# Performance work log

Measured on AMD Instinct MI355X. Metric: run time of the kernel, lower is better.

Reference implementation:

```python
import jax, jax.numpy as jnp
import numpy as np

CROP_H, CROP_W = 7, 7

def _sample_coords(lo, hi, extent, n):
    # TF crop_and_resize: coord = lo*(extent-1) + i*(hi-lo)*(extent-1)/(n-1)
    step = (hi - lo) * (extent - 1) / (n - 1)          # [N]
    return lo[:, None] * (extent - 1) + jnp.arange(n, dtype=lo.dtype)[None, :] * step[:, None]  # [N, n]

def crop_and_resize(image, boxes, box_ind, crop_h, crop_w):
    # image: [B,H,W,C], boxes: [N,4] normalized (y1,x1,y2,x2), box_ind: [N]
    B, H, W, C = image.shape
    y1, x1, y2, x2 = boxes[:, 0], boxes[:, 1], boxes[:, 2], boxes[:, 3]
    ys = _sample_coords(y1, y2, H, crop_h)             # [N, crop_h]
    xs = _sample_coords(x1, x2, W, crop_w)             # [N, crop_w]

    y0 = jnp.floor(ys); x0 = jnp.floor(xs)
    wy = (ys - y0)[:, :, None, None]                    # [N,ch,1,1] lerp weight
    wx = (xs - x0)[:, None, :, None]                    # [N,1,cw,1]
    y0i = jnp.clip(y0.astype(jnp.int32), 0, H - 1)
    y1i = jnp.clip(y0i + 1, 0, H - 1)
    x0i = jnp.clip(x0.astype(jnp.int32), 0, W - 1)
    x1i = jnp.clip(x0i + 1, 0, W - 1)

    b = box_ind[:, None, None]                          # [N,1,1]
    def corner(yi, xi):                                 # -> [N,ch,cw,C]
        return image[b, yi[:, :, None], xi[:, None, :]]

    top = corner(y0i, x0i) + (corner(y0i, x1i) - corner(y0i, x0i)) * wx
    bot = corner(y1i, x0i) + (corner(y1i, x1i) - corner(y1i, x0i)) * wx
    out = top + (bot - top) * wy                        # [N,ch,cw,C]

    # TF uses extrapolation_value=0 for samples outside the image
    vy = ((ys >= 0) & (ys <= H - 1))[:, :, None, None]
    vx = ((xs >= 0) & (xs <= W - 1))[:, None, :, None]
    return jnp.where(vy & vx, out, jnp.zeros((), out.dtype))


def setup_inputs() -> dict:
    key = jax.random.key(0)
    k1, k2, k3 = jax.random.split(key, 3)
    feats = jax.random.normal(k1, (8, 64, 64, 256), dtype=jnp.float32)
    boxes = jax.random.uniform(k2, (4000, 4), dtype=jnp.float32)
    box_ind = jax.random.randint(k3, (4000, 1), 0, 8, dtype=jnp.int32)
    return {"feats": feats, "boxes": boxes, "box_ind": box_ind}


def reference(feats, boxes, box_ind):
    ind = box_ind.reshape(-1)
    return crop_and_resize(feats, boxes, ind, CROP_H, CROP_W)
```

## Files before the change

kernel.cpp:

```cpp
#include <hip/hip_runtime.h>


#define H 64
#define W 64
#define C 256
#define CROP_HW 49
#define NIMG 8
#define G 8

typedef float f32x4 __attribute__((ext_vector_type(4)));

__global__ __launch_bounds__(512) void bucket_kernel(
    const int* __restrict__ box_ind,
    int* __restrict__ order,
    int* __restrict__ offsets,
    int n)
{
    const int wave = threadIdx.x >> 6;
    const int lane = threadIdx.x & 63;
    __shared__ int counts[NIMG];

    int cnt = 0;
    for (int i = lane; i < n; i += 64)
        cnt += (box_ind[i] == wave);
    for (int off = 32; off; off >>= 1)
        cnt += __shfl_down(cnt, off);
    if (lane == 0) counts[wave] = cnt;
    __syncthreads();

    int start = 0;
    for (int i = 0; i < wave; ++i) start += counts[i];
    if (threadIdx.x == 0) {
        int acc = 0;
        for (int i = 0; i < NIMG; ++i) { offsets[i] = acc; acc += counts[i]; }
        offsets[NIMG] = acc;
    }

    int pos = start;
    for (int base = 0; base < n; base += 64) {
        const int i = base + lane;
        const bool m = (i < n) && (box_ind[i] == wave);
        const unsigned long long mask = __ballot(m);
        const int below = __popcll(mask & ((1ULL << lane) - 1ULL));
        if (m) order[pos + below] = i;
        pos += __popcll(mask);
    }
}

struct Cell {
    int p00, p01, p10, p11;
    float wx, wy;
    bool valid;
    int oidx;
};

__device__ __forceinline__ Cell cell_info(
    int c, const int* __restrict__ order, const f32x4* __restrict__ boxes4,
    int start)
{
    Cell k;
    const int bi = c / CROP_HW;
    const int r  = c - bi * CROP_HW;
    const int iy = r / 7;
    const int ix = r - iy * 7;
    const int b  = order[start + bi];

    const f32x4 bx = boxes4[b];

    const float stepy = (bx.z - bx.x) * 63.0f / 6.0f;
    const float stepx = (bx.w - bx.y) * 63.0f / 6.0f;
    const float ys = bx.x * 63.0f + (float)iy * stepy;
    const float xs = bx.y * 63.0f + (float)ix * stepx;

    const float y0f = floorf(ys);
    const float x0f = floorf(xs);
    k.wy = ys - y0f;
    k.wx = xs - x0f;

    const int y0 = min(max((int)y0f, 0), H - 1);
    const int y1 = min(y0 + 1, H - 1);
    const int x0 = min(max((int)x0f, 0), W - 1);
    const int x1 = min(x0 + 1, W - 1);

    k.valid = (ys >= 0.0f) && (ys <= (float)(H - 1)) &&
              (xs >= 0.0f) && (xs <= (float)(W - 1));

    k.p00 = y0 * W + x0;
    k.p01 = y0 * W + x1;
    k.p10 = y1 * W + x0;
    k.p11 = y1 * W + x1;

    k.oidx = (b * CROP_HW + r) * (C / 4);
    return k;
}

__global__ __launch_bounds__(256, 4) void crop_resize_xcd(
    const float* __restrict__ feats,
    const float* __restrict__ boxes,
    const int*   __restrict__ order,
    const int*   __restrict__ offsets,
    float*       __restrict__ out)
{
    const int img  = blockIdx.x & 7;
    const int slot = blockIdx.x >> 3;
    const int lane = threadIdx.x & 63;
    const int wv   = threadIdx.x >> 6;

    const int start   = offsets[img];
    const int nb      = offsets[img + 1] - start;
    const int ncells  = nb * CROP_HW;
    const int ngroups = (ncells + G - 1) / G;
    const int wave_local = slot * 4 + wv;
    const int stride     = (gridDim.x >> 3) * 4;

    const f32x4* __restrict__ f4 = reinterpret_cast<const f32x4*>(feats)
                                   + (size_t)img * (H * W * (C / 4));
    const f32x4* __restrict__ boxes4 = reinterpret_cast<const f32x4*>(boxes);
    f32x4* __restrict__ o4 = reinterpret_cast<f32x4*>(out);

    for (int gi = wave_local; gi < ngroups; gi += stride) {
        const int cbase = gi * G;
        const int nval  = min(G, ncells - cbase);

        int c = cbase + (lane & (G - 1));
        if (c > ncells - 1) c = ncells - 1;
        const Cell k = cell_info(c, order, boxes4, start);
        const unsigned long long vmask = __ballot(k.valid);

        #pragma unroll
        for (int j = 0; j < G; ++j) {
            if (j >= nval) break;
            const int   s00 = __builtin_amdgcn_readlane(k.p00, j);
            const int   s01 = __builtin_amdgcn_readlane(k.p01, j);
            const int   s10 = __builtin_amdgcn_readlane(k.p10, j);
            const int   s11 = __builtin_amdgcn_readlane(k.p11, j);
            const float swx = __uint_as_float(
                __builtin_amdgcn_readlane(__float_as_uint(k.wx), j));
            const float swy = __uint_as_float(
                __builtin_amdgcn_readlane(__float_as_uint(k.wy), j));
            const int   sox = __builtin_amdgcn_readlane(k.oidx, j);
            const bool  sval = (vmask >> j) & 1ULL;

            const f32x4 v00 = f4[s00 * (C / 4) + lane];
            const f32x4 v01 = f4[s01 * (C / 4) + lane];
            const f32x4 v10 = f4[s10 * (C / 4) + lane];
            const f32x4 v11 = f4[s11 * (C / 4) + lane];

            const float w11 = swx * swy;
            const float w01 = swx - w11;
            const float w10 = swy - w11;
            const float w00 = 1.0f - swx - swy + w11;

            f32x4 res = v00 * w00;
            res += v01 * w01;
            res += v10 * w10;
            res += v11 * w11;
            if (!sval) res = (f32x4)0.0f;

            __builtin_nontemporal_store(res, &o4[sox + lane]);
        }
    }
}

extern "C" void kernel_launch(void* const* d_in, const int* in_sizes, int n_in,
                              void* d_out, int out_size, void* d_ws, size_t ws_size,
                              hipStream_t stream) {
    const float* feats   = (const float*)d_in[0];
    const float* boxes   = (const float*)d_in[1];
    const int*   box_ind = (const int*)d_in[2];
    float*       out     = (float*)d_out;

    const int n_boxes = in_sizes[1] / 4;

    int* order   = (int*)d_ws;
    int* offsets = order + n_boxes;

    bucket_kernel<<<1, 512, 0, stream>>>(box_ind, order, offsets, n_boxes);

    crop_resize_xcd<<<2048, 256, 0, stream>>>(feats, boxes, order, offsets, out);
}
```

Baseline: 70.38 us.

## Convert features to bf16 in a prep pass and gather from bf16 copy

```diff
diff --git a/kernel.cpp b/kernel.cpp
--- a/kernel.cpp
+++ b/kernel.cpp
@@ -8,42 +8,65 @@
 #define NIMG 8
 #define G 8
 
-typedef float f32x4 __attribute__((ext_vector_type(4)));
-
-__global__ __launch_bounds__(512) void bucket_kernel(
-    const int* __restrict__ box_ind,
+typedef float          f32x4 __attribute__((ext_vector_type(4)));
+typedef unsigned short u16x4 __attribute__((ext_vector_type(4)));
+typedef unsigned int   u32x2 __attribute__((ext_vector_type(2)));
+
+__device__ __forceinline__ unsigned short f2bf(float f) {
+    unsigned u = __float_as_uint(f);
+    unsigned r = (u + 0x7fffu + ((u >> 16) & 1u)) >> 16;
+    return (unsigned short)r;
+}
+
+__global__ __launch_bounds__(512) void prep_kernel(
+    const int*   __restrict__ box_ind,
+    const float* __restrict__ feats,
     int* __restrict__ order,
     int* __restrict__ offsets,
-    int n)
-{
-    const int wave = threadIdx.x >> 6;
-    const int lane = threadIdx.x & 63;
-    __shared__ int counts[NIMG];
-
-    int cnt = 0;
-    for (int i = lane; i < n; i += 64)
-        cnt += (box_ind[i] == wave);
-    for (int off = 32; off; off >>= 1)
-        cnt += __shfl_down(cnt, off);
-    if (lane == 0) counts[wave] = cnt;
-    __syncthreads();
-
-    int start = 0;
-    for (int i = 0; i < wave; ++i) start += counts[i];
-    if (threadIdx.x == 0) {
-        int acc = 0;
-        for (int i = 0; i < NIMG; ++i) { offsets[i] = acc; acc += counts[i]; }
-        offsets[NIMG] = acc;
-    }
-
-    int pos = start;
-    for (int base = 0; base < n; base += 64) {
-        const int i = base + lane;
-        const bool m = (i < n) && (box_ind[i] == wave);
-        const unsigned long long mask = __ballot(m);
-        const int below = __popcll(mask & ((1ULL << lane) - 1ULL));
-        if (m) order[pos + below] = i;
-        pos += __popcll(mask);
+    unsigned short* __restrict__ featsb,
+    int n, int n4)
+{
+    if (blockIdx.x == 0) {
+        const int wave = threadIdx.x >> 6;
+        const int lane = threadIdx.x & 63;
+        __shared__ int counts[NIMG];
+
+        int cnt = 0;
+        for (int i = lane; i < n; i += 64)
+            cnt += (box_ind[i] == wave);
+        for (int off = 32; off; off >>= 1)
+            cnt += __shfl_down(cnt, off);
+        if (lane == 0) counts[wave] = cnt;
+        __syncthreads();
+
+        int start = 0;
+        for (int i = 0; i < wave; ++i) start += counts[i];
+        if (threadIdx.x == 0) {
+            int acc = 0;
+            for (int i = 0; i < NIMG; ++i) { offsets[i] = acc; acc += counts[i]; }
+            offsets[NIMG] = acc;
+        }
+
+        int pos = start;
+        for (int base = 0; base < n; base += 64) {
+            const int i = base + lane;
+            const bool m = (i < n) && (box_ind[i] == wave);
+            const unsigned long long mask = __ballot(m);
+            const int below = __popcll(mask & ((1ULL << lane) - 1ULL));
+            if (m) order[pos + below] = i;
+            pos += __popcll(mask);
+        }
+    } else {
+        const f32x4* __restrict__ in4 = reinterpret_cast<const f32x4*>(feats);
+        u16x4* __restrict__ ob = reinterpret_cast<u16x4*>(featsb);
+        int i = (blockIdx.x - 1) * blockDim.x + threadIdx.x;
+        const int stride = (gridDim.x - 1) * blockDim.x;
+        for (; i < n4; i += stride) {
+            const f32x4 v = in4[i];
+            u16x4 r;
+            r.x = f2bf(v.x); r.y = f2bf(v.y); r.z = f2bf(v.z); r.w = f2bf(v.w);
+            ob[i] = r;
+        }
     }
 }
 
@@ -94,8 +117,17 @@
     return k;
 }
 
-__global__ __launch_bounds__(256, 4) void crop_resize_xcd(
-    const float* __restrict__ feats,
+__device__ __forceinline__ f32x4 bf4_to_f32(u32x2 u) {
+    f32x4 r;
+    r.x = __uint_as_float(u.x << 16);
+    r.y = __uint_as_float(u.x & 0xffff0000u);
+    r.z = __uint_as_float(u.y << 16);
+    r.w = __uint_as_float(u.y & 0xffff0000u);
+    return r;
+}
+
+__global__ __launch_bounds__(256, 4) void crop_resize_bf16(
+    const unsigned short* __restrict__ featsb,
     const float* __restrict__ boxes,
     const int*   __restrict__ order,
     const int*   __restrict__ offsets,
@@ -113,7 +145,7 @@
     const int wave_local = slot * 4 + wv;
     const int stride     = (gridDim.x >> 3) * 4;
 
-    const f32x4* __restrict__ f4 = reinterpret_cast<const f32x4*>(feats)
+    const u32x2* __restrict__ f2 = reinterpret_cast<const u32x2*>(featsb)
                                    + (size_t)img * (H * W * (C / 4));
     const f32x4* __restrict__ boxes4 = reinterpret_cast<const f32x4*>(boxes);
     f32x4* __restrict__ o4 = reinterpret_cast<f32x4*>(out);
@@ -141,6 +173,74 @@
             const int   sox = __builtin_amdgcn_readlane(k.oidx, j);
             const bool  sval = (vmask >> j) & 1ULL;
 
+            const u32x2 u00 = f2[s00 * (C / 4) + lane];
+            const u32x2 u01 = f2[s01 * (C / 4) + lane];
+            const u32x2 u10 = f2[s10 * (C / 4) + lane];
+            const u32x2 u11 = f2[s11 * (C / 4) + lane];
+
+            const float w11 = swx * swy;
+            const float w01 = swx - w11;
+            const float w10 = swy - w11;
+            const float w00 = 1.0f - swx - swy + w11;
+
+            f32x4 res = bf4_to_f32(u00) * w00;
+            res += bf4_to_f32(u01) * w01;
+            res += bf4_to_f32(u10) * w10;
+            res += bf4_to_f32(u11) * w11;
+            if (!sval) res = (f32x4)0.0f;
+
+            __builtin_nontemporal_store(res, &o4[(size_t)sox + lane]);
+        }
+    }
+}
+
+__global__ __launch_bounds__(256, 4) void crop_resize_f32(
+    const float* __restrict__ feats,
+    const float* __restrict__ boxes,
+    const int*   __restrict__ order,
+    const int*   __restrict__ offsets,
+    float*       __restrict__ out)
+{
+    const int img  = blockIdx.x & 7;
+    const int slot = blockIdx.x >> 3;
+    const int lane = threadIdx.x & 63;
+    const int wv   = threadIdx.x >> 6;
+
+    const int start   = offsets[img];
+    const int nb      = offsets[img + 1] - start;
+    const int ncells  = nb * CROP_HW;
+    const int ngroups = (ncells + G - 1) / G;
+    const int wave_local = slot * 4 + wv;
+    const int stride     = (gridDim.x >> 3) * 4;
+
+    const f32x4* __restrict__ f4 = reinterpret_cast<const f32x4*>(feats)
+                                   + (size_t)img * (H * W * (C / 4));
+    const f32x4* __restrict__ boxes4 = reinterpret_cast<const f32x4*>(boxes);
+    f32x4* __restrict__ o4 = reinterpret_cast<f32x4*>(out);
+
+    for (int gi = wave_local; gi < ngroups; gi += stride) {
+        const int cbase = gi * G;
+        const int nval  = min(G, ncells - cbase);
+
+        int c = cbase + (lane & (G - 1));
+        if (c > ncells - 1) c = ncells - 1;
+        const Cell k = cell_info(c, order, boxes4, start);
+        const unsigned long long vmask = __ballot(k.valid);
+
+        #pragma unroll
+        for (int j = 0; j < G; ++j) {
+            if (j >= nval) break;
+            const int   s00 = __builtin_amdgcn_readlane(k.p00, j);
+            const int   s01 = __builtin_amdgcn_readlane(k.p01, j);
+            const int   s10 = __builtin_amdgcn_readlane(k.p10, j);
+            const int   s11 = __builtin_amdgcn_readlane(k.p11, j);
+            const float swx = __uint_as_float(
+                __builtin_amdgcn_readlane(__float_as_uint(k.wx), j));
+            const float swy = __uint_as_float(
+                __builtin_amdgcn_readlane(__float_as_uint(k.wy), j));
+            const int   sox = __builtin_amdgcn_readlane(k.oidx, j);
+            const bool  sval = (vmask >> j) & 1ULL;
+
             const f32x4 v00 = f4[s00 * (C / 4) + lane];
             const f32x4 v01 = f4[s01 * (C / 4) + lane];
             const f32x4 v10 = f4[s10 * (C / 4) + lane];
@@ -157,7 +257,7 @@
             res += v11 * w11;
             if (!sval) res = (f32x4)0.0f;
 
-            __builtin_nontemporal_store(res, &o4[sox + lane]);
+            __builtin_nontemporal_store(res, &o4[(size_t)sox + lane]);
         }
     }
 }
@@ -171,11 +271,24 @@
     float*       out     = (float*)d_out;
 
     const int n_boxes = in_sizes[1] / 4;
+    const int n_feats = in_sizes[0];
 
     int* order   = (int*)d_ws;
     int* offsets = order + n_boxes;
-
-    bucket_kernel<<<1, 512, 0, stream>>>(box_ind, order, offsets, n_boxes);
-
-    crop_resize_xcd<<<2048, 256, 0, stream>>>(feats, boxes, order, offsets, out);
-}
+    const size_t bf_off   = 64 * 1024;
+    const size_t bf_bytes = (size_t)n_feats * 2;
+    unsigned short* featsb = (unsigned short*)((char*)d_ws + bf_off);
+
+    if (ws_size >= bf_off + bf_bytes) {
+        prep_kernel<<<1025, 512, 0, stream>>>(box_ind, feats, order, offsets,
+                                              featsb, n_boxes, n_feats / 4);
+        crop_resize_bf16<<<2048, 256, 0, stream>>>(featsb, boxes, order,
+                                                   offsets, out);
+    } else {
+        prep_kernel<<<1, 512, 0, stream>>>(box_ind, feats, order, offsets,
+                                           (unsigned short*)order ,
+                                           n_boxes, 0);
+        crop_resize_f32<<<2048, 256, 0, stream>>>(feats, boxes, order,
+                                                  offsets, out);
+    }
+}
```

Measured after the change: 73.97 us. 5.1% more time.

## Gather from packed bf16 horizontal-pair shadow and fuse bucketing into crop kernel

Applied to the files above, without the earlier changes.

```diff
diff --git a/kernel.cpp b/kernel.cpp
--- a/kernel.cpp
+++ b/kernel.cpp
@@ -7,63 +7,79 @@
 #define CROP_HW 49
 #define NIMG 8
 #define G 8
-
-typedef float f32x4 __attribute__((ext_vector_type(4)));
-
-__global__ __launch_bounds__(512) void bucket_kernel(
-    const int* __restrict__ box_ind,
-    int* __restrict__ order,
-    int* __restrict__ offsets,
-    int n)
-{
-    const int wave = threadIdx.x >> 6;
-    const int lane = threadIdx.x & 63;
-    __shared__ int counts[NIMG];
-
-    int cnt = 0;
-    for (int i = lane; i < n; i += 64)
-        cnt += (box_ind[i] == wave);
-    for (int off = 32; off; off >>= 1)
-        cnt += __shfl_down(cnt, off);
-    if (lane == 0) counts[wave] = cnt;
-    __syncthreads();
-
-    int start = 0;
-    for (int i = 0; i < wave; ++i) start += counts[i];
-    if (threadIdx.x == 0) {
-        int acc = 0;
-        for (int i = 0; i < NIMG; ++i) { offsets[i] = acc; acc += counts[i]; }
-        offsets[NIMG] = acc;
-    }
-
-    int pos = start;
-    for (int base = 0; base < n; base += 64) {
-        const int i = base + lane;
-        const bool m = (i < n) && (box_ind[i] == wave);
-        const unsigned long long mask = __ballot(m);
-        const int below = __popcll(mask & ((1ULL << lane) - 1ULL));
-        if (m) order[pos + below] = i;
-        pos += __popcll(mask);
+#define MAXB 4096
+
+typedef float        f32x4 __attribute__((ext_vector_type(4)));
+typedef unsigned int u32x4 __attribute__((ext_vector_type(4)));
+
+__device__ __forceinline__ unsigned f2bf(float f) {
+    const unsigned u = __float_as_uint(f);
+    return (u + 0x7fffu + ((u >> 16) & 1u)) >> 16;
+}
+__device__ __forceinline__ unsigned packpair(float a, float b) {
+    return f2bf(a) | (f2bf(b) << 16);
+}
+__device__ __forceinline__ f32x4 lopart(u32x4 u) {
+    f32x4 r;
+    r.x = __uint_as_float(u.x << 16);
+    r.y = __uint_as_float(u.y << 16);
+    r.z = __uint_as_float(u.z << 16);
+    r.w = __uint_as_float(u.w << 16);
+    return r;
+}
+__device__ __forceinline__ f32x4 hipart(u32x4 u) {
+    f32x4 r;
+    r.x = __uint_as_float(u.x & 0xffff0000u);
+    r.y = __uint_as_float(u.y & 0xffff0000u);
+    r.z = __uint_as_float(u.z & 0xffff0000u);
+    r.w = __uint_as_float(u.w & 0xffff0000u);
+    return r;
+}
+
+__global__ __launch_bounds__(256) void build_shadow(
+    const float* __restrict__ feats, unsigned int* __restrict__ shadow)
+{
+    const int img = blockIdx.x & 7;
+    const int blk = blockIdx.x >> 3;
+    const f32x4* __restrict__ in4 =
+        reinterpret_cast<const f32x4*>(feats) + (size_t)img * (H * W * (C / 4));
+    u32x4* __restrict__ o4 =
+        reinterpret_cast<u32x4*>(shadow) + (size_t)img * (H * W * (C / 4));
+
+    int t = blk * 1024 + threadIdx.x;
+    #pragma unroll
+    for (int it = 0; it < 4; ++it, t += 256) {
+        const int l   = t & (C / 4 - 1);
+        const int px  = t >> 6;
+        const int x   = px & (W - 1);
+        const int pxp = (x < W - 1) ? px + 1 : px;
+        const f32x4 a = in4[px  * (C / 4) + l];
+        const f32x4 b = in4[pxp * (C / 4) + l];
+        u32x4 r;
+        r.x = packpair(a.x, b.x);
+        r.y = packpair(a.y, b.y);
+        r.z = packpair(a.z, b.z);
+        r.w = packpair(a.w, b.w);
+        o4[t] = r;
     }
 }
 
 struct Cell {
-    int p00, p01, p10, p11;
+    int p0, p1;
     float wx, wy;
     bool valid;
     int oidx;
 };
 
 __device__ __forceinline__ Cell cell_info(
-    int c, const int* __restrict__ order, const f32x4* __restrict__ boxes4,
-    int start)
+    int c, const int* s_order, const f32x4* __restrict__ boxes4)
 {
     Cell k;
     const int bi = c / CROP_HW;
     const int r  = c - bi * CROP_HW;
     const int iy = r / 7;
     const int ix = r - iy * 7;
-    const int b  = order[start + bi];
+    const int b  = s_order[bi];
 
     const f32x4 bx = boxes4[b];
 
@@ -80,40 +96,59 @@
     const int y0 = min(max((int)y0f, 0), H - 1);
     const int y1 = min(y0 + 1, H - 1);
     const int x0 = min(max((int)x0f, 0), W - 1);
-    const int x1 = min(x0 + 1, W - 1);
 
     k.valid = (ys >= 0.0f) && (ys <= (float)(H - 1)) &&
               (xs >= 0.0f) && (xs <= (float)(W - 1));
 
-    k.p00 = y0 * W + x0;
-    k.p01 = y0 * W + x1;
-    k.p10 = y1 * W + x0;
-    k.p11 = y1 * W + x1;
+    k.p0 = y0 * W + x0;
+    k.p1 = y1 * W + x0;
 
     k.oidx = (b * CROP_HW + r) * (C / 4);
     return k;
 }
 
-__global__ __launch_bounds__(256, 4) void crop_resize_xcd(
-    const float* __restrict__ feats,
+__device__ __forceinline__ int block_bucket(
+    const int* __restrict__ box_ind, int nbox, int img, int lane, int wv,
+    int* s_order, int* s_nb)
+{
+    if (wv == 0) {
+        int pos = 0;
+        for (int base = 0; base < nbox; base += 64) {
+            const int i = base + lane;
+            const bool m = (i < nbox) && (box_ind[i] == img);
+            const unsigned long long mask = __ballot(m);
+            const int below = __popcll(mask & ((1ULL << lane) - 1ULL));
+            if (m) s_order[pos + below] = i;
+            pos += __popcll(mask);
+        }
+        if (lane == 0) *s_nb = pos;
+    }
+    __syncthreads();
+    return *s_nb;
+}
+
+__global__ __launch_bounds__(256, 4) void crop_pair(
+    const unsigned int* __restrict__ shadow,
     const float* __restrict__ boxes,
-    const int*   __restrict__ order,
-    const int*   __restrict__ offsets,
-    float*       __restrict__ out)
+    const int*   __restrict__ box_ind,
+    float*       __restrict__ out,
+    int nbox)
 {
     const int img  = blockIdx.x & 7;
     const int slot = blockIdx.x >> 3;
     const int lane = threadIdx.x & 63;
     const int wv   = threadIdx.x >> 6;
 
-    const int start   = offsets[img];
-    const int nb      = offsets[img + 1] - start;
+    __shared__ int s_order[MAXB];
+    __shared__ int s_nb;
+    const int nb = block_bucket(box_ind, nbox, img, lane, wv, s_order, &s_nb);
+
     const int ncells  = nb * CROP_HW;
     const int ngroups = (ncells + G - 1) / G;
     const int wave_local = slot * 4 + wv;
     const int stride     = (gridDim.x >> 3) * 4;
 
-    const f32x4* __restrict__ f4 = reinterpret_cast<const f32x4*>(feats)
+    const u32x4* __restrict__ pf = reinterpret_cast<const u32x4*>(shadow)
                                    + (size_t)img * (H * W * (C / 4));
     const f32x4* __restrict__ boxes4 = reinterpret_cast<const f32x4*>(boxes);
     f32x4* __restrict__ o4 = reinterpret_cast<f32x4*>(out);
@@ -124,16 +159,14 @@
 
         int c = cbase + (lane & (G - 1));
         if (c > ncells - 1) c = ncells - 1;
-        const Cell k = cell_info(c, order, boxes4, start);
+        const Cell k = cell_info(c, s_order, boxes4);
         const unsigned long long vmask = __ballot(k.valid);
 
         #pragma unroll
         for (int j = 0; j < G; ++j) {
             if (j >= nval) break;
-            const int   s00 = __builtin_amdgcn_readlane(k.p00, j);
-            const int   s01 = __builtin_amdgcn_readlane(k.p01, j);
-            const int   s10 = __builtin_amdgcn_readlane(k.p10, j);
-            const int   s11 = __builtin_amdgcn_readlane(k.p11, j);
+            const int   p0  = __builtin_amdgcn_readlane(k.p0, j);
+            const int   p1  = __builtin_amdgcn_readlane(k.p1, j);
             const float swx = __uint_as_float(
                 __builtin_amdgcn_readlane(__float_as_uint(k.wx), j));
             const float swy = __uint_as_float(
@@ -141,10 +174,80 @@
             const int   sox = __builtin_amdgcn_readlane(k.oidx, j);
             const bool  sval = (vmask >> j) & 1ULL;
 
-            const f32x4 v00 = f4[s00 * (C / 4) + lane];
-            const f32x4 v01 = f4[s01 * (C / 4) + lane];
-            const f32x4 v10 = f4[s10 * (C / 4) + lane];
-            const f32x4 v11 = f4[s11 * (C / 4) + lane];
+            const u32x4 r0 = pf[p0 * (C / 4) + lane];
+            const u32x4 r1 = pf[p1 * (C / 4) + lane];
+
+            const float w11 = swx * swy;
+            const float w01 = swx - w11;
+            const float w10 = swy - w11;
+            const float w00 = 1.0f - swx - swy + w11;
+
+            f32x4 res = lopart(r0) * w00;
+            res += hipart(r0) * w01;
+            res += lopart(r1) * w10;
+            res += hipart(r1) * w11;
+            if (!sval) res = (f32x4)0.0f;
+
+            __builtin_nontemporal_store(res, &o4[(size_t)sox + lane]);
+        }
+    }
+}
+
+__global__ __launch_bounds__(256, 4) void crop_f32(
+    const float* __restrict__ feats,
+    const float* __restrict__ boxes,
+    const int*   __restrict__ box_ind,
+    float*       __restrict__ out,
+    int nbox)
+{
+    const int img  = blockIdx.x & 7;
+    const int slot = blockIdx.x >> 3;
+    const int lane = threadIdx.x & 63;
+    const int wv   = threadIdx.x >> 6;
+
+    __shared__ int s_order[MAXB];
+    __shared__ int s_nb;
+    const int nb = block_bucket(box_ind, nbox, img, lane, wv, s_order, &s_nb);
+
+    const int ncells  = nb * CROP_HW;
+    const int ngroups = (ncells + G - 1) / G;
+    const int wave_local = slot * 4 + wv;
+    const int stride     = (gridDim.x >> 3) * 4;
+
+    const f32x4* __restrict__ f4 = reinterpret_cast<const f32x4*>(feats)
+                                   + (size_t)img * (H * W * (C / 4));
+    const f32x4* __restrict__ boxes4 = reinterpret_cast<const f32x4*>(boxes);
+    f32x4* __restrict__ o4 = reinterpret_cast<f32x4*>(out);
+
+    for (int gi = wave_local; gi < ngroups; gi += stride) {
+        const int cbase = gi * G;
+        const int nval  = min(G, ncells - cbase);
+
+        int c = cbase + (lane & (G - 1));
+        if (c > ncells - 1) c = ncells - 1;
+        const Cell k = cell_info(c, s_order, boxes4);
+        const unsigned long long vmask = __ballot(k.valid);
+
+        #pragma unroll
+        for (int j = 0; j < G; ++j) {
+            if (j >= nval) break;
+            const int   p0  = __builtin_amdgcn_readlane(k.p0, j);
+            const int   p1  = __builtin_amdgcn_readlane(k.p1, j);
+            const float swx = __uint_as_float(
+                __builtin_amdgcn_readlane(__float_as_uint(k.wx), j));
+            const float swy = __uint_as_float(
+                __builtin_amdgcn_readlane(__float_as_uint(k.wy), j));
+            const int   sox = __builtin_amdgcn_readlane(k.oidx, j);
+            const bool  sval = (vmask >> j) & 1ULL;
+
+            const int x00 = p0 & (W - 1);
+            const int p0b = (x00 < W - 1) ? p0 + 1 : p0;
+            const int p1b = (x00 < W - 1) ? p1 + 1 : p1;
+
+            const f32x4 v00 = f4[p0  * (C / 4) + lane];
+            const f32x4 v01 = f4[p0b * (C / 4) + lane];
+            const f32x4 v10 = f4[p1  * (C / 4) + lane];
+            const f32x4 v11 = f4[p1b * (C / 4) + lane];
 
             const float w11 = swx * swy;
             const float w01 = swx - w11;
@@ -157,7 +260,7 @@
             res += v11 * w11;
             if (!sval) res = (f32x4)0.0f;
 
-            __builtin_nontemporal_store(res, &o4[sox + lane]);
+            __builtin_nontemporal_store(res, &o4[(size_t)sox + lane]);
         }
     }
 }
@@ -171,11 +274,17 @@
     float*       out     = (float*)d_out;
 
     const int n_boxes = in_sizes[1] / 4;
-
-    int* order   = (int*)d_ws;
-    int* offsets = order + n_boxes;
-
-    bucket_kernel<<<1, 512, 0, stream>>>(box_ind, order, offsets, n_boxes);
-
-    crop_resize_xcd<<<2048, 256, 0, stream>>>(feats, boxes, order, offsets, out);
-}
+    const int n_feats = in_sizes[0];
+
+    const size_t shadow_bytes = (size_t)n_feats * 4;
+    unsigned int* shadow = (unsigned int*)d_ws;
+
+    if (n_boxes <= MAXB && ws_size >= shadow_bytes) {
+        build_shadow<<<2048, 256, 0, stream>>>(feats, shadow);
+        crop_pair<<<2048, 256, 0, stream>>>(shadow, boxes, box_ind, out, n_boxes);
+    } else if (n_boxes <= MAXB) {
+        crop_f32<<<2048, 256, 0, stream>>>(feats, boxes, box_ind, out, n_boxes);
+    } else {
+        crop_f32<<<2048, 256, 0, stream>>>(feats, boxes, box_ind, out, MAXB);
+    }
+}
```

After: 77.48 us. +10.1%, slower.

## Split block into producer waves computing and consumer waves storing via LDS

Applied to the files above, without the earlier changes.

```diff
diff --git a/kernel.cpp b/kernel.cpp
--- a/kernel.cpp
+++ b/kernel.cpp
@@ -6,7 +6,7 @@
 #define C 256
 #define CROP_HW 49
 #define NIMG 8
-#define G 8
+#define TILE 16
 
 typedef float f32x4 __attribute__((ext_vector_type(4)));
 
@@ -94,7 +94,7 @@
     return k;
 }
 
-__global__ __launch_bounds__(256, 4) void crop_resize_xcd(
+__global__ __launch_bounds__(256, 4) void crop_pc(
     const float* __restrict__ feats,
     const float* __restrict__ boxes,
     const int*   __restrict__ order,
@@ -106,59 +106,76 @@
     const int lane = threadIdx.x & 63;
     const int wv   = threadIdx.x >> 6;
 
-    const int start   = offsets[img];
-    const int nb      = offsets[img + 1] - start;
-    const int ncells  = nb * CROP_HW;
-    const int ngroups = (ncells + G - 1) / G;
-    const int wave_local = slot * 4 + wv;
-    const int stride     = (gridDim.x >> 3) * 4;
+    const int start  = offsets[img];
+    const int nb     = offsets[img + 1] - start;
+    const int ncells = nb * CROP_HW;
+    const int ntiles = (ncells + TILE - 1) / TILE;
+    const int nslots = gridDim.x >> 3;
 
     const f32x4* __restrict__ f4 = reinterpret_cast<const f32x4*>(feats)
                                    + (size_t)img * (H * W * (C / 4));
     const f32x4* __restrict__ boxes4 = reinterpret_cast<const f32x4*>(boxes);
     f32x4* __restrict__ o4 = reinterpret_cast<f32x4*>(out);
 
-    for (int gi = wave_local; gi < ngroups; gi += stride) {
-        const int cbase = gi * G;
-        const int nval  = min(G, ncells - cbase);
+    __shared__ f32x4 buf[TILE][64];
+    __shared__ int   oid[TILE];
 
-        int c = cbase + (lane & (G - 1));
-        if (c > ncells - 1) c = ncells - 1;
-        const Cell k = cell_info(c, order, boxes4, start);
-        const unsigned long long vmask = __ballot(k.valid);
+    for (int t = slot; t < ntiles; t += nslots) {
+        const int cbase = t * TILE;
 
-        #pragma unroll
-        for (int j = 0; j < G; ++j) {
-            if (j >= nval) break;
-            const int   s00 = __builtin_amdgcn_readlane(k.p00, j);
-            const int   s01 = __builtin_amdgcn_readlane(k.p01, j);
-            const int   s10 = __builtin_amdgcn_readlane(k.p10, j);
-            const int   s11 = __builtin_amdgcn_readlane(k.p11, j);
-            const float swx = __uint_as_float(
-                __builtin_amdgcn_readlane(__float_as_uint(k.wx), j));
-            const float swy = __uint_as_float(
-                __builtin_amdgcn_readlane(__float_as_uint(k.wy), j));
-            const int   sox = __builtin_amdgcn_readlane(k.oidx, j);
-            const bool  sval = (vmask >> j) & 1ULL;
+        if (wv < 2) {
+            int c = cbase + wv * 8 + (lane & 7);
+            if (c > ncells - 1) c = ncells - 1;
+            const Cell k = cell_info(c, order, boxes4, start);
+            const unsigned long long vmask = __ballot(k.valid);
 
-            const f32x4 v00 = f4[s00 * (C / 4) + lane];
-            const f32x4 v01 = f4[s01 * (C / 4) + lane];
-            const f32x4 v10 = f4[s10 * (C / 4) + lane];
-            const f32x4 v11 = f4[s11 * (C / 4) + lane];
+            if (lane < 8) oid[wv * 8 + lane] = k.oidx;
 
-            const float w11 = swx * swy;
-            const float w01 = swx - w11;
-            const float w10 = swy - w11;
-            const float w00 = 1.0f - swx - swy + w11;
+            #pragma unroll
+            for (int j = 0; j < 8; ++j) {
+                const int   s00 = __builtin_amdgcn_readlane(k.p00, j);
+                const int   s01 = __builtin_amdgcn_readlane(k.p01, j);
+                const int   s10 = __builtin_amdgcn_readlane(k.p10, j);
+                const int   s11 = __builtin_amdgcn_readlane(k.p11, j);
+                const float swx = __uint_as_float(
+                    __builtin_amdgcn_readlane(__float_as_uint(k.wx), j));
+                const float swy = __uint_as_float(
+                    __builtin_amdgcn_readlane(__float_as_uint(k.wy), j));
+                const bool  sval = (vmask >> j) & 1ULL;
 
-            f32x4 res = v00 * w00;
-            res += v01 * w01;
-            res += v10 * w10;
-            res += v11 * w11;
-            if (!sval) res = (f32x4)0.0f;
+                const f32x4 v00 = f4[s00 * (C / 4) + lane];
+                const f32x4 v01 = f4[s01 * (C / 4) + lane];
+                const f32x4 v10 = f4[s10 * (C / 4) + lane];
+                const f32x4 v11 = f4[s11 * (C / 4) + lane];
 
-            __builtin_nontemporal_store(res, &o4[sox + lane]);
+                const float w11 = swx * swy;
+                const float w01 = swx - w11;
+                const float w10 = swy - w11;
+                const float w00 = 1.0f - swx - swy + w11;
+
+                f32x4 res = v00 * w00;
+                res += v01 * w01;
+                res += v10 * w10;
+                res += v11 * w11;
+                if (!sval) res = (f32x4)0.0f;
+
+                buf[wv * 8 + j][lane] = res;
+            }
         }
+
+        __syncthreads();
+
+        if (wv >= 2) {
+            #pragma unroll
+            for (int j = 0; j < 8; ++j) {
+                const int row = (wv - 2) * 8 + j;
+                const f32x4 res = buf[row][lane];
+                const int   ox  = oid[row];
+                __builtin_nontemporal_store(res, &o4[(size_t)ox + lane]);
+            }
+        }
+
+        __syncthreads();
     }
 }
 
@@ -177,5 +194,5 @@
 
     bucket_kernel<<<1, 512, 0, stream>>>(box_ind, order, offsets, n_boxes);
 
-    crop_resize_xcd<<<2048, 256, 0, stream>>>(feats, boxes, order, offsets, out);
+    crop_pc<<<2048, 256, 0, stream>>>(feats, boxes, order, offsets, out);
 }
```

After: 74.69 us. 1.06x slower.
